# Kernel tuning notes

Hardware: AMD Instinct MI355X
Metric: run time of the kernel (lower is better)

Reference implementation:

```python
import jax, jax.numpy as jnp
import numpy as np

B, N, C, F, O = 32, 2048, 8, 128, 128


def setup_inputs() -> dict:
    key = jax.random.key(0)
    k1, k2, k3, k4, k5, k6 = jax.random.split(key, 6)
    nodes = jax.random.normal(k1, (B, N, F), dtype=jnp.float32)
    children = jax.random.randint(k2, (B, N, C), 0, N, dtype=jnp.int32)
    w_t = jax.random.normal(k3, (F, O), dtype=jnp.float32) * 0.05
    w_l = jax.random.normal(k4, (F, O), dtype=jnp.float32) * 0.05
    w_r = jax.random.normal(k5, (F, O), dtype=jnp.float32) * 0.05
    b = jax.random.normal(k6, (O,), dtype=jnp.float32) * 0.05
    return {"nodes": nodes, "children": children, "w_t": w_t, "w_l": w_l, "w_r": w_r, "b": b}


def reference(nodes, children, w_t, w_l, w_r, b):
    Bb, Nn, Ff = nodes.shape
    Cc = children.shape[2]
    dt = nodes.dtype

    # --- children tensor: index 0 maps to zero vector ---
    lookup = jnp.concatenate([jnp.zeros((Bb, 1, Ff), dt), nodes[:, 1:, :]], axis=1)
    batch_idx = jnp.arange(Bb)[:, None, None]
    child_vecs = lookup[batch_idx, children]                      # [B,N,C,F]
    tree = jnp.concatenate([nodes[:, :, None, :], child_vecs], axis=2)  # [B,N,C+1,F]

    # --- coefficients ---
    ch_f = children.astype(dt)
    c_t = jnp.broadcast_to(
        jnp.concatenate([jnp.ones((1, 1, 1), dt), jnp.zeros((1, 1, Cc), dt)], axis=2),
        (Bb, Nn, Cc + 1))                                          # [B,N,C+1]
    num_sib = jnp.count_nonzero(children, axis=2, keepdims=True).astype(dt)  # [B,N,1]
    mask = jnp.concatenate(
        [jnp.zeros((Bb, Nn, 1), dt), jnp.minimum(ch_f, 1.0)], axis=2)        # [B,N,C+1]
    child_indices = jnp.arange(-1.0, Cc, 1.0, dtype=dt)[None, None, :] * mask
    singles = jnp.concatenate(
        [jnp.zeros((Bb, Nn, 1), dt),
         jnp.full((Bb, Nn, 1), 0.5, dt),
         jnp.zeros((Bb, Nn, Cc - 1), dt)], axis=2)
    is_single = num_sib == 1.0
    denom = jnp.where(is_single, 1.0, num_sib - 1.0)  # safe divide, matches tf.where select
    c_r = jnp.where(is_single, singles, (1.0 - c_t) * (child_indices / denom))
    c_l = (1.0 - c_t) * (1.0 - c_r) * mask
    coef = jnp.stack([c_t, c_r, c_l], axis=3)                      # [B,N,C+1,3]

    # --- weighted aggregation + small GEMM ---
    agg = jnp.einsum('bncf,bnck->bnkf', tree, coef)                # [B,N,3,F]
    w = jnp.stack([w_t, w_r, w_l], axis=0)                         # [3,F,O]
    out = jnp.einsum('bnkf,kfo->bno', agg, w)
    return jax.nn.relu(out + b)
```

## Files before the change

kernel.cpp:

```cpp
#include <hip/hip_runtime.h>

typedef unsigned short ushort_t;
typedef __attribute__((ext_vector_type(8))) short short8;
typedef __attribute__((ext_vector_type(4))) short short4v;
typedef __attribute__((ext_vector_type(4))) float float4v;

#define Bn 32
#define Nn 2048
#define Cn 8
#define Fn 128
#define On 128
#define Kn 384
#define MT 32
#define LDSK 392

__device__ __forceinline__ ushort_t f2bf(float x) {
  unsigned u = __float_as_uint(x);
  u += 0x7fffu + ((u >> 16) & 1u);
  return (ushort_t)(u >> 16);
}

__global__ void prep_w_kernel(const float* __restrict__ w_t,
                              const float* __restrict__ w_l,
                              const float* __restrict__ w_r,
                              ushort_t* __restrict__ wsw) {
  int t = blockIdx.x * blockDim.x + threadIdx.x;
  if (t >= 6144) return;
  int lane = t & 63;
  int r = t >> 6;
  int ks = r % 12;
  int q = r / 12;
  int ct = q & 1;
  int w = q >> 1;
  int col = w * 32 + ct * 16 + (lane & 15);
  int kbase = ((lane >> 4) * 8) + ks * 32;
  ushort_t* dst = wsw + (size_t)t * 8;
#pragma unroll
  for (int j = 0; j < 8; ++j) {
    int k = kbase + j;
    const float* src = (k < Fn) ? w_t : (k < 2 * Fn) ? w_r : w_l;
    int f = k & (Fn - 1);
    dst[j] = f2bf(src[f * On + col]);
  }
}

__global__ __launch_bounds__(256)
void tree_conv_kernel(const float* __restrict__ nodes,
                      const int* __restrict__ children,
                      const ushort_t* __restrict__ wsw,
                      const float* __restrict__ bias,
                      float* __restrict__ out) {
  __shared__ __align__(16) ushort_t agg[MT * LDSK];

  const int tid = threadIdx.x;

  const int sb = ((blockIdx.x & 7) << 8) | (blockIdx.x >> 3);

  {
    const int grp = tid >> 5;
    const int ln = tid & 31;

#pragma unroll
    for (int it = 0; it < 4; ++it) {
      const int row = it * 8 + grp;
      const int g = sb * MT + row;
      const int base_row = g & ~(Nn - 1);

      const int4* chv = (const int4*)(children + (size_t)g * Cn);
      int4 ca = chv[0], cb = chv[1];
      int idx[Cn] = {ca.x, ca.y, ca.z, ca.w, cb.x, cb.y, cb.z, cb.w};

      int ns = 0;
#pragma unroll
      for (int c = 0; c < Cn; ++c) ns += (idx[c] != 0);
      const float denom = (ns > 1) ? (float)(ns - 1) : 1.0f;

      float crv[Cn], clv[Cn];
#pragma unroll
      for (int c = 0; c < Cn; ++c) {
        float m = (idx[c] != 0) ? 1.0f : 0.0f;
        float cr0 = (ns == 1) ? ((c == 0) ? 0.5f : 0.0f) : ((float)c / denom);
        float cr = cr0 * m;
        crv[c] = cr;
        clv[c] = (1.0f - cr) * m;
        idx[c] &= (Nn - 1);
      }

      const float4v sv = *((const float4v*)(nodes + (size_t)g * Fn) + ln);

      float4v rr = {0.f, 0.f, 0.f, 0.f};
      float4v ll = {0.f, 0.f, 0.f, 0.f};
#pragma unroll
      for (int c = 0; c < Cn; ++c) {
        const float4v v =
            *((const float4v*)(nodes + (size_t)(base_row + idx[c]) * Fn) + ln);
        rr += crv[c] * v;
        ll += clv[c] * v;
      }

      ushort_t* arow = agg + row * LDSK;
      short4v ps = {(short)f2bf(sv.x), (short)f2bf(sv.y),
                    (short)f2bf(sv.z), (short)f2bf(sv.w)};
      short4v pr = {(short)f2bf(rr.x), (short)f2bf(rr.y),
                    (short)f2bf(rr.z), (short)f2bf(rr.w)};
      short4v pl = {(short)f2bf(ll.x), (short)f2bf(ll.y),
                    (short)f2bf(ll.z), (short)f2bf(ll.w)};
      *(short4v*)(arow + ln * 4) = ps;
      *(short4v*)(arow + Fn + ln * 4) = pr;
      *(short4v*)(arow + 2 * Fn + ln * 4) = pl;
    }
  }

  __syncthreads();

  const int lane = tid & 63;
  const int wave = tid >> 6;
  const int l15 = lane & 15;
  const int quad = lane >> 4;

#pragma unroll
  for (int ct = 0; ct < 2; ++ct) {
    const short8* bp = (const short8*)wsw + ((wave * 2 + ct) * 12) * 64 + lane;
    short8 bfrag[12];
#pragma unroll
    for (int ks = 0; ks < 12; ++ks) bfrag[ks] = bp[ks * 64];

    const int col = wave * 32 + ct * 16 + l15;
    const float bb = bias[col];

#pragma unroll
    for (int st = 0; st < 2; ++st) {
      const ushort_t* ar = agg + (st * 16 + l15) * LDSK + quad * 8;
      float4v acc = {0.f, 0.f, 0.f, 0.f};
#pragma unroll
      for (int ks = 0; ks < 12; ++ks) {
        short8 af = *(const short8*)(ar + ks * 32);
        acc = __builtin_amdgcn_mfma_f32_16x16x32_bf16(af, bfrag[ks], acc, 0, 0, 0);
      }
      const int grow0 = sb * MT + st * 16 + quad * 4;
#pragma unroll
      for (int r2 = 0; r2 < 4; ++r2) {
        out[(size_t)(grow0 + r2) * On + col] = fmaxf(acc[r2] + bb, 0.f);
      }
    }
  }
}

extern "C" void kernel_launch(void* const* d_in, const int* in_sizes, int n_in,
                              void* d_out, int out_size, void* d_ws, size_t ws_size,
                              hipStream_t stream) {
  const float* nodes = (const float*)d_in[0];
  const int* children = (const int*)d_in[1];
  const float* w_t = (const float*)d_in[2];
  const float* w_l = (const float*)d_in[3];
  const float* w_r = (const float*)d_in[4];
  const float* bias = (const float*)d_in[5];
  float* out = (float*)d_out;
  ushort_t* wsw = (ushort_t*)d_ws;

  prep_w_kernel<<<24, 256, 0, stream>>>(w_t, w_l, w_r, wsw);
  tree_conv_kernel<<<(Bn * Nn) / MT, 256, 0, stream>>>(nodes, children, wsw, bias, out);
}
```

Measured before the change: 122.9 us.

## Make tree conv persistent with double-buffered gather and precomputed coefficients

Rewrites the main kernel to use 512 blocks of 512 threads. Each block processes 8 tiles of 16 rows, with double-buffered LDS so the gather for the next tile overlaps the MFMA of the current one. The B fragments stay in registers for the whole block lifetime. Child coefficients are now computed in a separate prep kernel and staged through LDS, which adds one extra launch and a global round-trip for the coefficients.

```diff
diff --git a/kernel.cpp b/kernel.cpp
--- a/kernel.cpp
+++ b/kernel.cpp
@@ -3,6 +3,7 @@
 typedef unsigned short ushort_t;
 typedef __attribute__((ext_vector_type(8))) short short8;
 typedef __attribute__((ext_vector_type(4))) short short4v;
+typedef __attribute__((ext_vector_type(2))) float float2v;
 typedef __attribute__((ext_vector_type(4))) float float4v;
 
 #define Bn 32
@@ -11,8 +12,10 @@
 #define Fn 128
 #define On 128
 #define Kn 384
-#define MT 32
+#define MT 16
+#define NT 8
 #define LDSK 392
+#define NBLK 512
 
 __device__ __forceinline__ ushort_t f2bf(float x) {
   unsigned u = __float_as_uint(x);
@@ -30,9 +33,7 @@
   int r = t >> 6;
   int ks = r % 12;
   int q = r / 12;
-  int ct = q & 1;
-  int w = q >> 1;
-  int col = w * 32 + ct * 16 + (lane & 15);
+  int col = q * 16 + (lane & 15);
   int kbase = ((lane >> 4) * 8) + ks * 32;
   ushort_t* dst = wsw + (size_t)t * 8;
 #pragma unroll
@@ -44,105 +45,133 @@
   }
 }
 
-__global__ __launch_bounds__(256)
+__global__ void prep_coef_kernel(const int* __restrict__ children,
+                                 float* __restrict__ coef) {
+  int g = blockIdx.x * blockDim.x + threadIdx.x;
+  if (g >= Bn * Nn) return;
+  const int4* chv = (const int4*)(children + (size_t)g * Cn);
+  int4 ca = chv[0], cb = chv[1];
+  int idx[Cn] = {ca.x, ca.y, ca.z, ca.w, cb.x, cb.y, cb.z, cb.w};
+  int ns = 0;
+#pragma unroll
+  for (int c = 0; c < Cn; ++c) ns += (idx[c] != 0);
+  const float denom = (ns > 1) ? (float)(ns - 1) : 1.0f;
+  float o[16];
+#pragma unroll
+  for (int c = 0; c < Cn; ++c) {
+    float m = (idx[c] != 0) ? 1.0f : 0.0f;
+    float cr0 = (ns == 1) ? ((c == 0) ? 0.5f : 0.0f) : ((float)c / denom);
+    float cr = cr0 * m;
+    o[2 * c] = cr;
+    o[2 * c + 1] = (1.0f - cr) * m;
+  }
+  float4v* dst = (float4v*)(coef + (size_t)g * 16);
+#pragma unroll
+  for (int j = 0; j < 4; ++j) {
+    float4v v = {o[4 * j], o[4 * j + 1], o[4 * j + 2], o[4 * j + 3]};
+    dst[j] = v;
+  }
+}
+
+__global__ __launch_bounds__(512, 4)
 void tree_conv_kernel(const float* __restrict__ nodes,
                       const int* __restrict__ children,
+                      const float* __restrict__ coefb,
                       const ushort_t* __restrict__ wsw,
                       const float* __restrict__ bias,
                       float* __restrict__ out) {
-  __shared__ __align__(16) ushort_t agg[MT * LDSK];
+  __shared__ __align__(16) ushort_t agg[2][MT * LDSK];
+  __shared__ __align__(16) int ch_lds[NT * MT * Cn];
+  __shared__ __align__(16) float cf_lds[NT * MT * 16];
 
   const int tid = threadIdx.x;
+  const int wave = tid >> 6;
+  const int lane = tid & 63;
+  const int l15 = lane & 15;
+  const int quad = lane >> 4;
+  const int grp = tid >> 5;
+  const int ln = tid & 31;
 
-  const int sb = ((blockIdx.x & 7) << 8) | (blockIdx.x >> 3);
+  const int sb = ((blockIdx.x & 7) << 6) | (blockIdx.x >> 3);
+  const int rb0 = sb * (MT * NT);
+  const int batch_base = rb0 & ~(Nn - 1);
 
+  if (tid < 256)
+    ((int4*)ch_lds)[tid] = ((const int4*)(children + (size_t)rb0 * Cn))[tid];
+  ((float4v*)cf_lds)[tid] = ((const float4v*)(coefb + (size_t)rb0 * 16))[tid];
+
+  short8 bfrag[12];
   {
-    const int grp = tid >> 5;
-    const int ln = tid & 31;
-
+    const short8* bp = (const short8*)wsw + (wave * 12) * 64 + lane;
 #pragma unroll
-    for (int it = 0; it < 4; ++it) {
-      const int row = it * 8 + grp;
-      const int g = sb * MT + row;
-      const int base_row = g & ~(Nn - 1);
-
-      const int4* chv = (const int4*)(children + (size_t)g * Cn);
-      int4 ca = chv[0], cb = chv[1];
-      int idx[Cn] = {ca.x, ca.y, ca.z, ca.w, cb.x, cb.y, cb.z, cb.w};
-
-      int ns = 0;
-#pragma unroll
-      for (int c = 0; c < Cn; ++c) ns += (idx[c] != 0);
-      const float denom = (ns > 1) ? (float)(ns - 1) : 1.0f;
-
-      float crv[Cn], clv[Cn];
-#pragma unroll
-      for (int c = 0; c < Cn; ++c) {
-        float m = (idx[c] != 0) ? 1.0f : 0.0f;
-        float cr0 = (ns == 1) ? ((c == 0) ? 0.5f : 0.0f) : ((float)c / denom);
-        float cr = cr0 * m;
-        crv[c] = cr;
-        clv[c] = (1.0f - cr) * m;
-        idx[c] &= (Nn - 1);
-      }
-
-      const float4v sv = *((const float4v*)(nodes + (size_t)g * Fn) + ln);
-
-      float4v rr = {0.f, 0.f, 0.f, 0.f};
-      float4v ll = {0.f, 0.f, 0.f, 0.f};
-#pragma unroll
-      for (int c = 0; c < Cn; ++c) {
-        const float4v v =
-            *((const float4v*)(nodes + (size_t)(base_row + idx[c]) * Fn) + ln);
-        rr += crv[c] * v;
-        ll += clv[c] * v;
-      }
-
-      ushort_t* arow = agg + row * LDSK;
-      short4v ps = {(short)f2bf(sv.x), (short)f2bf(sv.y),
-                    (short)f2bf(sv.z), (short)f2bf(sv.w)};
-      short4v pr = {(short)f2bf(rr.x), (short)f2bf(rr.y),
-                    (short)f2bf(rr.z), (short)f2bf(rr.w)};
-      short4v pl = {(short)f2bf(ll.x), (short)f2bf(ll.y),
-                    (short)f2bf(ll.z), (short)f2bf(ll.w)};
-      *(short4v*)(arow + ln * 4) = ps;
-      *(short4v*)(arow + Fn + ln * 4) = pr;
-      *(short4v*)(arow + 2 * Fn + ln * 4) = pl;
-    }
+    for (int ks = 0; ks < 12; ++ks) bfrag[ks] = bp[ks * 64];
   }
+  const int col = wave * 16 + l15;
+  const float bb = bias[col];
 
   __syncthreads();
 
-  const int lane = tid & 63;
-  const int wave = tid >> 6;
-  const int l15 = lane & 15;
-  const int quad = lane >> 4;
+  float4v gv[Cn], sv, cf[4];
 
+  auto issue = [&](int t) {
+    const int lrow = t * MT + grp;
+    int4 ia = ((const int4*)(ch_lds + lrow * Cn))[0];
+    int4 ib = ((const int4*)(ch_lds + lrow * Cn))[1];
+    const float4v* cp = (const float4v*)(cf_lds + lrow * 16);
+    cf[0] = cp[0]; cf[1] = cp[1]; cf[2] = cp[2]; cf[3] = cp[3];
+    const int g = rb0 + lrow;
+    sv = *((const float4v*)(nodes + (size_t)g * Fn) + ln);
+    int idx[Cn] = {ia.x, ia.y, ia.z, ia.w, ib.x, ib.y, ib.z, ib.w};
 #pragma unroll
-  for (int ct = 0; ct < 2; ++ct) {
-    const short8* bp = (const short8*)wsw + ((wave * 2 + ct) * 12) * 64 + lane;
-    short8 bfrag[12];
+    for (int c = 0; c < Cn; ++c) {
+      const int r = batch_base + (idx[c] & (Nn - 1));
+      gv[c] = *((const float4v*)(nodes + (size_t)r * Fn) + ln);
+    }
+  };
+
+  auto combine = [&](int buf) {
+    float2v rl0 = {0.f, 0.f}, rl1 = {0.f, 0.f}, rl2 = {0.f, 0.f}, rl3 = {0.f, 0.f};
 #pragma unroll
-    for (int ks = 0; ks < 12; ++ks) bfrag[ks] = bp[ks * 64];
+    for (int c = 0; c < Cn; ++c) {
+      const float2v cc = {cf[c >> 1][(c & 1) * 2], cf[c >> 1][(c & 1) * 2 + 1]};
+      const float4v v = gv[c];
+      rl0 += (float2v){v.x, v.x} * cc;
+      rl1 += (float2v){v.y, v.y} * cc;
+      rl2 += (float2v){v.z, v.z} * cc;
+      rl3 += (float2v){v.w, v.w} * cc;
+    }
+    ushort_t* arow = agg[buf] + grp * LDSK;
+    short4v ps = {(short)f2bf(sv.x), (short)f2bf(sv.y),
+                  (short)f2bf(sv.z), (short)f2bf(sv.w)};
+    short4v pr = {(short)f2bf(rl0.x), (short)f2bf(rl1.x),
+                  (short)f2bf(rl2.x), (short)f2bf(rl3.x)};
+    short4v pl = {(short)f2bf(rl0.y), (short)f2bf(rl1.y),
+                  (short)f2bf(rl2.y), (short)f2bf(rl3.y)};
+    *(short4v*)(arow + ln * 4) = ps;
+    *(short4v*)(arow + Fn + ln * 4) = pr;
+    *(short4v*)(arow + 2 * Fn + ln * 4) = pl;
+  };
 
-    const int col = wave * 32 + ct * 16 + l15;
-    const float bb = bias[col];
+  issue(0);
+  combine(0);
 
+  for (int t = 0; t < NT; ++t) {
+    __syncthreads();
+    if (t + 1 < NT) issue(t + 1);
+
+    const ushort_t* ar = agg[t & 1] + l15 * LDSK + quad * 8;
+    float4v acc = {0.f, 0.f, 0.f, 0.f};
 #pragma unroll
-    for (int st = 0; st < 2; ++st) {
-      const ushort_t* ar = agg + (st * 16 + l15) * LDSK + quad * 8;
-      float4v acc = {0.f, 0.f, 0.f, 0.f};
+    for (int ks = 0; ks < 12; ++ks) {
+      short8 af = *(const short8*)(ar + ks * 32);
+      acc = __builtin_amdgcn_mfma_f32_16x16x32_bf16(af, bfrag[ks], acc, 0, 0, 0);
+    }
+    const int grow = rb0 + t * MT + quad * 4;
 #pragma unroll
-      for (int ks = 0; ks < 12; ++ks) {
-        short8 af = *(const short8*)(ar + ks * 32);
-        acc = __builtin_amdgcn_mfma_f32_16x16x32_bf16(af, bfrag[ks], acc, 0, 0, 0);
-      }
-      const int grow0 = sb * MT + st * 16 + quad * 4;
-#pragma unroll
-      for (int r2 = 0; r2 < 4; ++r2) {
-        out[(size_t)(grow0 + r2) * On + col] = fmaxf(acc[r2] + bb, 0.f);
-      }
-    }
+    for (int r2 = 0; r2 < 4; ++r2)
+      out[(size_t)(grow + r2) * On + col] = fmaxf(acc[r2] + bb, 0.f);
+
+    if (t + 1 < NT) combine((t + 1) & 1);
   }
 }
 
@@ -156,8 +185,11 @@
   const float* w_r = (const float*)d_in[4];
   const float* bias = (const float*)d_in[5];
   float* out = (float*)d_out;
-  ushort_t* wsw = (ushort_t*)d_ws;
+
+  float* coefb = (float*)d_ws;
+  ushort_t* wsw = (ushort_t*)((char*)d_ws + (4u << 20));
 
   prep_w_kernel<<<24, 256, 0, stream>>>(w_t, w_l, w_r, wsw);
-  tree_conv_kernel<<<(Bn * Nn) / MT, 256, 0, stream>>>(nodes, children, wsw, bias, out);
+  prep_coef_kernel<<<(Bn * Nn) / 256, 256, 0, stream>>>(children, coefb);
+  tree_conv_kernel<<<NBLK, 512, 0, stream>>>(nodes, children, coefb, wsw, bias, out);
 }
```

Measured after the change: 120.3 us. -2.1%, faster.

## Split fused gather-GEMM kernel into gather pass and MFMA GEMM pass via workspace

Applied to the files above, without the earlier changes.

Splits the single fused kernel in two. The first kernel gathers the children, computes the coefficients once per row in LDS, and writes the bf16 aggregated rows to a global workspace, using small 8-row blocks for more parallelism on the gather. The second kernel loads 64-row tiles into LDS and runs the MFMA GEMM, with each wave keeping both column tiles of weights in registers. The aim is to decouple the latency-bound gather from the GEMM and improve weight-fragment reuse, at the cost of an extra global write and read of about 50MB of intermediate data plus another kernel launch.

```diff
diff --git a/kernel.cpp b/kernel.cpp
--- a/kernel.cpp
+++ b/kernel.cpp
@@ -3,6 +3,7 @@
 typedef unsigned short ushort_t;
 typedef __attribute__((ext_vector_type(8))) short short8;
 typedef __attribute__((ext_vector_type(4))) short short4v;
+typedef __attribute__((ext_vector_type(2))) float float2v;
 typedef __attribute__((ext_vector_type(4))) float float4v;
 
 #define Bn 32
@@ -10,9 +11,9 @@
 #define Cn 8
 #define Fn 128
 #define On 128
-#define Kn 384
-#define MT 32
-#define LDSK 392
+#define AGGK 392
+#define P1ROWS 8
+#define P2ROWS 64
 
 __device__ __forceinline__ ushort_t f2bf(float x) {
   unsigned u = __float_as_uint(x);
@@ -30,9 +31,7 @@
   int r = t >> 6;
   int ks = r % 12;
   int q = r / 12;
-  int ct = q & 1;
-  int w = q >> 1;
-  int col = w * 32 + ct * 16 + (lane & 15);
+  int col = q * 16 + (lane & 15);
   int kbase = ((lane >> 4) * 8) + ks * 32;
   ushort_t* dst = wsw + (size_t)t * 8;
 #pragma unroll
@@ -45,103 +44,133 @@
 }
 
 __global__ __launch_bounds__(256)
-void tree_conv_kernel(const float* __restrict__ nodes,
-                      const int* __restrict__ children,
-                      const ushort_t* __restrict__ wsw,
-                      const float* __restrict__ bias,
-                      float* __restrict__ out) {
-  __shared__ __align__(16) ushort_t agg[MT * LDSK];
+void pass1_kernel(const float* __restrict__ nodes,
+                  const int* __restrict__ children,
+                  ushort_t* __restrict__ agg) {
+  __shared__ int ch_lds[P1ROWS * Cn];
+  __shared__ float cf_lds[P1ROWS * 16];
 
   const int tid = threadIdx.x;
+  const int sb = ((blockIdx.x & 7) << 10) | (blockIdx.x >> 3);
+  const int rb0 = sb * P1ROWS;
 
-  const int sb = ((blockIdx.x & 7) << 8) | (blockIdx.x >> 3);
+  if (tid < P1ROWS * Cn / 4)
+    ((int4*)ch_lds)[tid] = ((const int4*)(children + (size_t)rb0 * Cn))[tid];
+  __syncthreads();
 
-  {
-    const int grp = tid >> 5;
-    const int ln = tid & 31;
-
+  if (tid < P1ROWS) {
+    const int* ch = ch_lds + tid * Cn;
+    int idx[Cn];
 #pragma unroll
-    for (int it = 0; it < 4; ++it) {
-      const int row = it * 8 + grp;
-      const int g = sb * MT + row;
-      const int base_row = g & ~(Nn - 1);
-
-      const int4* chv = (const int4*)(children + (size_t)g * Cn);
-      int4 ca = chv[0], cb = chv[1];
-      int idx[Cn] = {ca.x, ca.y, ca.z, ca.w, cb.x, cb.y, cb.z, cb.w};
-
-      int ns = 0;
+    for (int c = 0; c < Cn; ++c) idx[c] = ch[c];
+    int ns = 0;
 #pragma unroll
-      for (int c = 0; c < Cn; ++c) ns += (idx[c] != 0);
-      const float denom = (ns > 1) ? (float)(ns - 1) : 1.0f;
-
-      float crv[Cn], clv[Cn];
+    for (int c = 0; c < Cn; ++c) ns += (idx[c] != 0);
+    const float denom = (ns > 1) ? (float)(ns - 1) : 1.0f;
 #pragma unroll
-      for (int c = 0; c < Cn; ++c) {
-        float m = (idx[c] != 0) ? 1.0f : 0.0f;
-        float cr0 = (ns == 1) ? ((c == 0) ? 0.5f : 0.0f) : ((float)c / denom);
-        float cr = cr0 * m;
-        crv[c] = cr;
-        clv[c] = (1.0f - cr) * m;
-        idx[c] &= (Nn - 1);
-      }
-
-      const float4v sv = *((const float4v*)(nodes + (size_t)g * Fn) + ln);
-
-      float4v rr = {0.f, 0.f, 0.f, 0.f};
-      float4v ll = {0.f, 0.f, 0.f, 0.f};
-#pragma unroll
-      for (int c = 0; c < Cn; ++c) {
-        const float4v v =
-            *((const float4v*)(nodes + (size_t)(base_row + idx[c]) * Fn) + ln);
-        rr += crv[c] * v;
-        ll += clv[c] * v;
-      }
-
-      ushort_t* arow = agg + row * LDSK;
-      short4v ps = {(short)f2bf(sv.x), (short)f2bf(sv.y),
-                    (short)f2bf(sv.z), (short)f2bf(sv.w)};
-      short4v pr = {(short)f2bf(rr.x), (short)f2bf(rr.y),
-                    (short)f2bf(rr.z), (short)f2bf(rr.w)};
-      short4v pl = {(short)f2bf(ll.x), (short)f2bf(ll.y),
-                    (short)f2bf(ll.z), (short)f2bf(ll.w)};
-      *(short4v*)(arow + ln * 4) = ps;
-      *(short4v*)(arow + Fn + ln * 4) = pr;
-      *(short4v*)(arow + 2 * Fn + ln * 4) = pl;
+    for (int c = 0; c < Cn; ++c) {
+      float m = (idx[c] != 0) ? 1.0f : 0.0f;
+      float cr0 = (ns == 1) ? ((c == 0) ? 0.5f : 0.0f) : ((float)c / denom);
+      float cr = cr0 * m;
+      cf_lds[tid * 16 + 2 * c] = cr;
+      cf_lds[tid * 16 + 2 * c + 1] = (1.0f - cr) * m;
     }
   }
-
   __syncthreads();
 
+  const int grp = tid >> 5;
+  const int ln = tid & 31;
+  const int g = rb0 + grp;
+  const int base_row = g & ~(Nn - 1);
+
+  const float4v sv = *((const float4v*)(nodes + (size_t)g * Fn) + ln);
+
+  float4v gv[Cn];
+#pragma unroll
+  for (int c = 0; c < Cn; ++c) {
+    const int r = base_row + (ch_lds[grp * Cn + c] & (Nn - 1));
+    gv[c] = *((const float4v*)(nodes + (size_t)r * Fn) + ln);
+  }
+
+  float2v rl0 = {0.f, 0.f}, rl1 = {0.f, 0.f}, rl2 = {0.f, 0.f}, rl3 = {0.f, 0.f};
+#pragma unroll
+  for (int c = 0; c < Cn; ++c) {
+    const float2v cc = {cf_lds[grp * 16 + 2 * c], cf_lds[grp * 16 + 2 * c + 1]};
+    const float4v v = gv[c];
+    rl0 += (float2v){v.x, v.x} * cc;
+    rl1 += (float2v){v.y, v.y} * cc;
+    rl2 += (float2v){v.z, v.z} * cc;
+    rl3 += (float2v){v.w, v.w} * cc;
+  }
+
+  ushort_t* arow = agg + (size_t)g * AGGK;
+  short4v ps = {(short)f2bf(sv.x), (short)f2bf(sv.y),
+                (short)f2bf(sv.z), (short)f2bf(sv.w)};
+  short4v pr = {(short)f2bf(rl0.x), (short)f2bf(rl1.x),
+                (short)f2bf(rl2.x), (short)f2bf(rl3.x)};
+  short4v pl = {(short)f2bf(rl0.y), (short)f2bf(rl1.y),
+                (short)f2bf(rl2.y), (short)f2bf(rl3.y)};
+  *(short4v*)(arow + ln * 4) = ps;
+  *(short4v*)(arow + Fn + ln * 4) = pr;
+  *(short4v*)(arow + 2 * Fn + ln * 4) = pl;
+}
+
+__global__ __launch_bounds__(256)
+void pass2_kernel(const ushort_t* __restrict__ agg,
+                  const ushort_t* __restrict__ wsw,
+                  const float* __restrict__ bias,
+                  float* __restrict__ out) {
+  __shared__ __align__(16) ushort_t tile[P2ROWS * AGGK];
+
+  const int tid = threadIdx.x;
+  const int rb0 = blockIdx.x * P2ROWS;
   const int lane = tid & 63;
   const int wave = tid >> 6;
   const int l15 = lane & 15;
   const int quad = lane >> 4;
 
+  const short8* gsrc = (const short8*)(agg + (size_t)rb0 * AGGK);
+  short8 sreg[12];
 #pragma unroll
-  for (int ct = 0; ct < 2; ++ct) {
-    const short8* bp = (const short8*)wsw + ((wave * 2 + ct) * 12) * 64 + lane;
-    short8 bfrag[12];
+  for (int it = 0; it < 12; ++it) sreg[it] = gsrc[it * 256 + tid];
+  short8 srem;
+  if (tid < 64) srem = gsrc[3072 + tid];
+
+  short8* ldst = (short8*)tile;
 #pragma unroll
-    for (int ks = 0; ks < 12; ++ks) bfrag[ks] = bp[ks * 64];
+  for (int it = 0; it < 12; ++it) ldst[it * 256 + tid] = sreg[it];
+  if (tid < 64) ldst[3072 + tid] = srem;
 
-    const int col = wave * 32 + ct * 16 + l15;
-    const float bb = bias[col];
+  short8 bfrag[2][12];
+#pragma unroll
+  for (int ct = 0; ct < 2; ++ct)
+#pragma unroll
+    for (int ks = 0; ks < 12; ++ks)
+      bfrag[ct][ks] =
+          ((const short8*)wsw)[(((wave * 2 + ct) * 12) + ks) * 64 + lane];
+
+  const int col0 = wave * 32 + l15;
+  const float bb0 = bias[col0];
+  const float bb1 = bias[col0 + 16];
+
+  __syncthreads();
 
 #pragma unroll
-    for (int st = 0; st < 2; ++st) {
-      const ushort_t* ar = agg + (st * 16 + l15) * LDSK + quad * 8;
-      float4v acc = {0.f, 0.f, 0.f, 0.f};
+  for (int st4 = 0; st4 < 4; ++st4) {
+    const ushort_t* ar = tile + (st4 * 16 + l15) * AGGK + quad * 8;
+    float4v acc0 = {0.f, 0.f, 0.f, 0.f};
+    float4v acc1 = {0.f, 0.f, 0.f, 0.f};
 #pragma unroll
-      for (int ks = 0; ks < 12; ++ks) {
-        short8 af = *(const short8*)(ar + ks * 32);
-        acc = __builtin_amdgcn_mfma_f32_16x16x32_bf16(af, bfrag[ks], acc, 0, 0, 0);
-      }
-      const int grow0 = sb * MT + st * 16 + quad * 4;
+    for (int ks = 0; ks < 12; ++ks) {
+      short8 af = *(const short8*)(ar + ks * 32);
+      acc0 = __builtin_amdgcn_mfma_f32_16x16x32_bf16(af, bfrag[0][ks], acc0, 0, 0, 0);
+      acc1 = __builtin_amdgcn_mfma_f32_16x16x32_bf16(af, bfrag[1][ks], acc1, 0, 0, 0);
+    }
+    const int grow = rb0 + st4 * 16 + quad * 4;
 #pragma unroll
-      for (int r2 = 0; r2 < 4; ++r2) {
-        out[(size_t)(grow0 + r2) * On + col] = fmaxf(acc[r2] + bb, 0.f);
-      }
+    for (int r2 = 0; r2 < 4; ++r2) {
+      out[(size_t)(grow + r2) * On + col0] = fmaxf(acc0[r2] + bb0, 0.f);
+      out[(size_t)(grow + r2) * On + col0 + 16] = fmaxf(acc1[r2] + bb1, 0.f);
     }
   }
 }
@@ -156,8 +185,11 @@
   const float* w_r = (const float*)d_in[4];
   const float* bias = (const float*)d_in[5];
   float* out = (float*)d_out;
-  ushort_t* wsw = (ushort_t*)d_ws;
+
+  ushort_t* agg = (ushort_t*)d_ws;
+  ushort_t* wsw = (ushort_t*)((char*)d_ws + ((size_t)64 << 20));
 
   prep_w_kernel<<<24, 256, 0, stream>>>(w_t, w_l, w_r, wsw);
-  tree_conv_kernel<<<(Bn * Nn) / MT, 256, 0, stream>>>(nodes, children, wsw, bias, out);
+  pass1_kernel<<<(Bn * Nn) / P1ROWS, 256, 0, stream>>>(nodes, children, agg);
+  pass2_kernel<<<(Bn * Nn) / P2ROWS, 256, 0, stream>>>(agg, wsw, bias, out);
 }
```

Result: slower. 127.2 us (+3.4%).

## Split fused tree conv into coefficient prep, gather pass, and MFMA GEMM pass

Applied to the files above, without the earlier changes.

Splits the single fused kernel into three launches. A prep kernel computes the per-node child coefficients alongside the weight swizzle. A gather pass writes bf16 aggregates to global memory in an MFMA-ready tiled layout, using one node per 32 threads for more parallelism. A GEMM pass streams each tile into LDS with global_load_lds and runs the MFMAs. The aim is to decouple the latency-bound gather from the GEMM so each runs at better occupancy, at the cost of a ~50MB global round trip and extra launches.

```diff
diff --git a/kernel.cpp b/kernel.cpp
--- a/kernel.cpp
+++ b/kernel.cpp
@@ -1,8 +1,10 @@
 #include <hip/hip_runtime.h>
 
 typedef unsigned short ushort_t;
+typedef unsigned int uint_t;
 typedef __attribute__((ext_vector_type(8))) short short8;
-typedef __attribute__((ext_vector_type(4))) short short4v;
+typedef __attribute__((ext_vector_type(2))) uint_t uint2v;
+typedef __attribute__((ext_vector_type(2))) float float2v;
 typedef __attribute__((ext_vector_type(4))) float float4v;
 
 #define Bn 32
@@ -10,9 +12,7 @@
 #define Cn 8
 #define Fn 128
 #define On 128
-#define Kn 384
-#define MT 32
-#define LDSK 392
+#define TILE_SHORTS (32 * 384)
 
 __device__ __forceinline__ ushort_t f2bf(float x) {
   unsigned u = __float_as_uint(x);
@@ -20,128 +20,158 @@
   return (ushort_t)(u >> 16);
 }
 
-__global__ void prep_w_kernel(const float* __restrict__ w_t,
-                              const float* __restrict__ w_l,
-                              const float* __restrict__ w_r,
-                              ushort_t* __restrict__ wsw) {
-  int t = blockIdx.x * blockDim.x + threadIdx.x;
-  if (t >= 6144) return;
-  int lane = t & 63;
-  int r = t >> 6;
-  int ks = r % 12;
-  int q = r / 12;
-  int ct = q & 1;
-  int w = q >> 1;
-  int col = w * 32 + ct * 16 + (lane & 15);
-  int kbase = ((lane >> 4) * 8) + ks * 32;
-  ushort_t* dst = wsw + (size_t)t * 8;
+__device__ __forceinline__ uint_t pk2bf(float lo, float hi) {
+  return __builtin_amdgcn_perm(__float_as_uint(hi), __float_as_uint(lo),
+                               0x07060302u);
+}
+
+__global__ __launch_bounds__(256)
+void prep_kernel(const float* __restrict__ w_t, const float* __restrict__ w_l,
+                 const float* __restrict__ w_r, const int* __restrict__ children,
+                 ushort_t* __restrict__ wsw, float* __restrict__ coefb) {
+  if (blockIdx.x < 24) {
+    int t = blockIdx.x * 256 + threadIdx.x;
+    int lane = t & 63;
+    int r = t >> 6;
+    int ks = r % 12;
+    int q = r / 12;
+    int col = q * 16 + (lane & 15);
+    int kbase = ((lane >> 4) * 8) + ks * 32;
+    ushort_t* dst = wsw + (size_t)t * 8;
 #pragma unroll
-  for (int j = 0; j < 8; ++j) {
-    int k = kbase + j;
-    const float* src = (k < Fn) ? w_t : (k < 2 * Fn) ? w_r : w_l;
-    int f = k & (Fn - 1);
-    dst[j] = f2bf(src[f * On + col]);
+    for (int j = 0; j < 8; ++j) {
+      int k = kbase + j;
+      const float* src = (k < Fn) ? w_t : (k < 2 * Fn) ? w_r : w_l;
+      int f = k & (Fn - 1);
+      dst[j] = f2bf(src[f * On + col]);
+    }
+  } else {
+    int g = (blockIdx.x - 24) * 256 + threadIdx.x;
+    const int4* chv = (const int4*)(children + (size_t)g * Cn);
+    int4 ca = chv[0], cb = chv[1];
+    int idx[Cn] = {ca.x, ca.y, ca.z, ca.w, cb.x, cb.y, cb.z, cb.w};
+    int ns = 0;
+#pragma unroll
+    for (int c = 0; c < Cn; ++c) ns += (idx[c] != 0);
+    const float denom = (ns > 1) ? (float)(ns - 1) : 1.0f;
+    float o[16];
+#pragma unroll
+    for (int c = 0; c < Cn; ++c) {
+      float m = (idx[c] != 0) ? 1.0f : 0.0f;
+      float cr0 = (ns == 1) ? ((c == 0) ? 0.5f : 0.0f) : ((float)c / denom);
+      float cr = cr0 * m;
+      o[2 * c] = cr;
+      o[2 * c + 1] = (1.0f - cr) * m;
+    }
+    float4v* dst = (float4v*)(coefb + (size_t)g * 16);
+#pragma unroll
+    for (int j = 0; j < 4; ++j) {
+      float4v v = {o[4 * j], o[4 * j + 1], o[4 * j + 2], o[4 * j + 3]};
+      dst[j] = v;
+    }
   }
 }
 
 __global__ __launch_bounds__(256)
-void tree_conv_kernel(const float* __restrict__ nodes,
-                      const int* __restrict__ children,
-                      const ushort_t* __restrict__ wsw,
-                      const float* __restrict__ bias,
-                      float* __restrict__ out) {
-  __shared__ __align__(16) ushort_t agg[MT * LDSK];
+void pass1_kernel(const float* __restrict__ nodes,
+                  const int* __restrict__ children,
+                  const float* __restrict__ coefb,
+                  ushort_t* __restrict__ agg) {
+  const int tid = threadIdx.x;
+  const int sb = ((blockIdx.x & 7) << 10) | (blockIdx.x >> 3);
+  const int rb0 = sb * 8;
+  const int g = rb0 + (tid >> 5);
+  const int ln = tid & 31;
+  const int batch_row0 = rb0 & ~(Nn - 1);
+  const float* nb = nodes + (size_t)batch_row0 * Fn;
+
+  const int4* chv = (const int4*)(children + (size_t)g * Cn);
+  int4 ca = chv[0], cb = chv[1];
+  const float4v* cfp = (const float4v*)(coefb + (size_t)g * 16);
+  float4v cf[4] = {cfp[0], cfp[1], cfp[2], cfp[3]};
+
+  const float4v sv = *((const float4v*)(nodes + (size_t)g * Fn) + ln);
+
+  int idx[Cn] = {ca.x, ca.y, ca.z, ca.w, cb.x, cb.y, cb.z, cb.w};
+  float4v gv[Cn];
+#pragma unroll
+  for (int c = 0; c < Cn; ++c) {
+    gv[c] = *((const float4v*)(nb + (size_t)(idx[c] & (Nn - 1)) * Fn) + ln);
+  }
+
+  float2v rl0 = {0.f, 0.f}, rl1 = {0.f, 0.f}, rl2 = {0.f, 0.f}, rl3 = {0.f, 0.f};
+#pragma unroll
+  for (int c = 0; c < Cn; ++c) {
+    const float2v cc = {cf[c >> 1][(c & 1) * 2], cf[c >> 1][(c & 1) * 2 + 1]};
+    const float4v v = gv[c];
+    rl0 += (float2v){v.x, v.x} * cc;
+    rl1 += (float2v){v.y, v.y} * cc;
+    rl2 += (float2v){v.z, v.z} * cc;
+    rl3 += (float2v){v.w, v.w} * cc;
+  }
+
+  ushort_t* ap = agg + (size_t)(g >> 5) * TILE_SHORTS + (g & 31) * 8 + (ln & 1) * 4;
+  const int ub = (ln >> 1) * 256;
+  *(uint2v*)(ap + ub) = (uint2v){pk2bf(sv.x, sv.y), pk2bf(sv.z, sv.w)};
+  *(uint2v*)(ap + ub + 16 * 256) =
+      (uint2v){pk2bf(rl0.x, rl1.x), pk2bf(rl2.x, rl3.x)};
+  *(uint2v*)(ap + ub + 32 * 256) =
+      (uint2v){pk2bf(rl0.y, rl1.y), pk2bf(rl2.y, rl3.y)};
+}
+
+__global__ __launch_bounds__(256)
+void pass2_kernel(const ushort_t* __restrict__ agg,
+                  const ushort_t* __restrict__ wsw,
+                  const float* __restrict__ bias,
+                  float* __restrict__ out) {
+  __shared__ __align__(16) ushort_t tile[TILE_SHORTS];
 
   const int tid = threadIdx.x;
+  const int lane = tid & 63;
+  const int wave = tid >> 6;
+  const int l15 = lane & 15;
+  const int quad = lane >> 4;
+  const int b = ((blockIdx.x & 7) << 8) | (blockIdx.x >> 3);
+  const int rb0 = b * 32;
 
-  const int sb = ((blockIdx.x & 7) << 8) | (blockIdx.x >> 3);
-
-  {
-    const int grp = tid >> 5;
-    const int ln = tid & 31;
-
+  const uint_t* gsrc = (const uint_t*)(agg + (size_t)b * TILE_SHORTS);
 #pragma unroll
-    for (int it = 0; it < 4; ++it) {
-      const int row = it * 8 + grp;
-      const int g = sb * MT + row;
-      const int base_row = g & ~(Nn - 1);
-
-      const int4* chv = (const int4*)(children + (size_t)g * Cn);
-      int4 ca = chv[0], cb = chv[1];
-      int idx[Cn] = {ca.x, ca.y, ca.z, ca.w, cb.x, cb.y, cb.z, cb.w};
-
-      int ns = 0;
-#pragma unroll
-      for (int c = 0; c < Cn; ++c) ns += (idx[c] != 0);
-      const float denom = (ns > 1) ? (float)(ns - 1) : 1.0f;
-
-      float crv[Cn], clv[Cn];
-#pragma unroll
-      for (int c = 0; c < Cn; ++c) {
-        float m = (idx[c] != 0) ? 1.0f : 0.0f;
-        float cr0 = (ns == 1) ? ((c == 0) ? 0.5f : 0.0f) : ((float)c / denom);
-        float cr = cr0 * m;
-        crv[c] = cr;
-        clv[c] = (1.0f - cr) * m;
-        idx[c] &= (Nn - 1);
-      }
-
-      const float4v sv = *((const float4v*)(nodes + (size_t)g * Fn) + ln);
-
-      float4v rr = {0.f, 0.f, 0.f, 0.f};
-      float4v ll = {0.f, 0.f, 0.f, 0.f};
-#pragma unroll
-      for (int c = 0; c < Cn; ++c) {
-        const float4v v =
-            *((const float4v*)(nodes + (size_t)(base_row + idx[c]) * Fn) + ln);
-        rr += crv[c] * v;
-        ll += clv[c] * v;
-      }
-
-      ushort_t* arow = agg + row * LDSK;
-      short4v ps = {(short)f2bf(sv.x), (short)f2bf(sv.y),
-                    (short)f2bf(sv.z), (short)f2bf(sv.w)};
-      short4v pr = {(short)f2bf(rr.x), (short)f2bf(rr.y),
-                    (short)f2bf(rr.z), (short)f2bf(rr.w)};
-      short4v pl = {(short)f2bf(ll.x), (short)f2bf(ll.y),
-                    (short)f2bf(ll.z), (short)f2bf(ll.w)};
-      *(short4v*)(arow + ln * 4) = ps;
-      *(short4v*)(arow + Fn + ln * 4) = pr;
-      *(short4v*)(arow + 2 * Fn + ln * 4) = pl;
-    }
+  for (int it = 0; it < 6; ++it) {
+    const int unit1k = wave * 6 + it;
+    __builtin_amdgcn_global_load_lds(
+        (const __attribute__((address_space(1))) uint_t*)(gsrc + unit1k * 256 +
+                                                          lane * 4),
+        (__attribute__((address_space(3))) uint_t*)(uint_t*)(void*)(
+            tile + unit1k * 512),
+        16, 0, 0);
   }
 
   __syncthreads();
 
-  const int lane = tid & 63;
-  const int wave = tid >> 6;
-  const int l15 = lane & 15;
-  const int quad = lane >> 4;
-
 #pragma unroll
   for (int ct = 0; ct < 2; ++ct) {
-    const short8* bp = (const short8*)wsw + ((wave * 2 + ct) * 12) * 64 + lane;
+    const int q = wave * 2 + ct;
     short8 bfrag[12];
 #pragma unroll
-    for (int ks = 0; ks < 12; ++ks) bfrag[ks] = bp[ks * 64];
+    for (int ks = 0; ks < 12; ++ks)
+      bfrag[ks] = ((const short8*)wsw)[(q * 12 + ks) * 64 + lane];
 
-    const int col = wave * 32 + ct * 16 + l15;
+    const int col = q * 16 + l15;
     const float bb = bias[col];
 
 #pragma unroll
     for (int st = 0; st < 2; ++st) {
-      const ushort_t* ar = agg + (st * 16 + l15) * LDSK + quad * 8;
       float4v acc = {0.f, 0.f, 0.f, 0.f};
 #pragma unroll
       for (int ks = 0; ks < 12; ++ks) {
-        short8 af = *(const short8*)(ar + ks * 32);
+        const short8 af =
+            *(const short8*)(tile + ((ks * 4 + quad) * 32 + st * 16 + l15) * 8);
         acc = __builtin_amdgcn_mfma_f32_16x16x32_bf16(af, bfrag[ks], acc, 0, 0, 0);
       }
-      const int grow0 = sb * MT + st * 16 + quad * 4;
+      const int grow = rb0 + st * 16 + quad * 4;
 #pragma unroll
-      for (int r2 = 0; r2 < 4; ++r2) {
-        out[(size_t)(grow0 + r2) * On + col] = fmaxf(acc[r2] + bb, 0.f);
-      }
+      for (int r2 = 0; r2 < 4; ++r2)
+        out[(size_t)(grow + r2) * On + col] = fmaxf(acc[r2] + bb, 0.f);
     }
   }
 }
@@ -156,8 +186,12 @@
   const float* w_r = (const float*)d_in[4];
   const float* bias = (const float*)d_in[5];
   float* out = (float*)d_out;
-  ushort_t* wsw = (ushort_t*)d_ws;
 
-  prep_w_kernel<<<24, 256, 0, stream>>>(w_t, w_l, w_r, wsw);
-  tree_conv_kernel<<<(Bn * Nn) / MT, 256, 0, stream>>>(nodes, children, wsw, bias, out);
+  ushort_t* agg = (ushort_t*)d_ws;
+  ushort_t* wsw = (ushort_t*)((char*)d_ws + ((size_t)64 << 20));
+  float* coefb = (float*)((char*)d_ws + ((size_t)80 << 20));
+
+  prep_kernel<<<280, 256, 0, stream>>>(w_t, w_l, w_r, children, wsw, coefb);
+  pass1_kernel<<<(Bn * Nn) / 8, 256, 0, stream>>>(nodes, children, coefb, agg);
+  pass2_kernel<<<(Bn * Nn) / 32, 256, 0, stream>>>(agg, wsw, bias, out);
 }
```

New measurement: 136.7 us. 11.2% more time.
